# Optimization experiments

Measured on AMD Instinct MI355X. Metric: run time of the kernel, lower is better.

## Reference

```python
import jax, jax.numpy as jnp
import numpy as np

B, S, D, H, E = 4, 1024, 1024, 16, 4
HD = D // H
EPS = 1e-5


def setup_inputs() -> dict:
    key = jax.random.key(0)
    ks = jax.random.split(key, 6)
    std = 0.02
    return {
        "hidden_states": jax.random.normal(ks[0], (B, S, D), dtype=jnp.float32),
        "Wr": jax.random.normal(ks[1], (D, E), dtype=jnp.float32) * std,
        "br": jnp.zeros((E,), jnp.float32),
        "ln_g": jnp.ones((E, D), jnp.float32),
        "ln_b": jnp.zeros((E, D), jnp.float32),
        "W_attn": jax.random.normal(ks[2], (E, D, 3 * D), dtype=jnp.float32) * std,
        "b_attn": jnp.zeros((E, 3 * D), jnp.float32),
        "W_proj": jax.random.normal(ks[3], (E, D, D), dtype=jnp.float32) * std,
        "b_proj": jnp.zeros((E, D), jnp.float32),
    }


def reference(hidden_states, Wr, br, ln_g, ln_b, W_attn, b_attn, W_proj, b_proj):
    b, s, d = hidden_states.shape
    x = hidden_states.reshape(b * s, d)  # [N, D]

    # naive softmax router over experts
    score = jax.nn.softmax(x @ Wr + br, axis=-1)  # [N, E]

    # LayerNorm stats are expert-independent; affine is per-expert
    mu = jnp.mean(x, axis=-1, keepdims=True)
    var = jnp.mean(jnp.square(x - mu), axis=-1, keepdims=True)
    xn = (x - mu) * jax.lax.rsqrt(var + EPS)  # [N, D]

    ln_out = xn[:, None, :] * ln_g[None] + ln_b[None]  # [N, E, D]
    qkv_all = jnp.einsum('ned,edf->nef', ln_out, W_attn) + b_attn  # [N, E, 3D]
    # weighted_qkv: scale each expert's qkv by its routing score, sum
    qkv = jnp.einsum('ne,nef->nf', score, qkv_all)  # [N, 3D]

    q, k, v = jnp.split(qkv.reshape(b, s, 3 * d), 3, axis=-1)
    def split_heads(t):
        return t.reshape(b, s, H, HD).transpose(0, 2, 1, 3)  # [B,H,S,hd]
    q, k, v = split_heads(q), split_heads(k), split_heads(v)

    scale = 1.0 / jnp.sqrt(jnp.asarray(HD, q.dtype))
    att = jnp.einsum('bhqd,bhkd->bhqk', q, k) * scale  # [B,H,S,S]
    causal = jnp.tril(jnp.ones((s, s), dtype=bool))
    att = jnp.where(causal[None, None], att, jnp.finfo(att.dtype).min)
    probs = jax.nn.softmax(att, axis=-1)
    ctx = jnp.einsum('bhqk,bhkd->bhqd', probs, v)  # [B,H,S,hd]
    ctx = ctx.transpose(0, 2, 1, 3).reshape(b * s, d)  # [N, D]

    proj_all = jnp.einsum('nd,edf->nef', ctx, W_proj) + b_proj  # [N, E, D]
    out = jnp.einsum('ne,nef->nf', score, proj_all).reshape(b, s, d)
    return out
```

## Files before the change

kernel.cpp:

```cpp
#include <hip/hip_runtime.h>
#include <stdint.h>

#define NB 4
#define SS 1024
#define DD 1024
#define EE 4
#define HH 16
#define HDD 64
#define NN (NB*SS)
#define KK2 (EE*DD)
#define FF1 (3*DD)

typedef __attribute__((ext_vector_type(4))) float f32x4;
typedef __attribute__((ext_vector_type(8))) _Float16 half8;
typedef __attribute__((ext_vector_type(4))) _Float16 half4;

static __device__ __forceinline__ f32x4 mfma16(half8 a, half8 b, f32x4 c){
  return __builtin_amdgcn_mfma_f32_16x16x32_f16(a, b, c, 0, 0, 0);
}

#define GLOAD_LDS16(gp, lp) __builtin_amdgcn_global_load_lds( \
    (const unsigned int __attribute__((address_space(1)))*)(uintptr_t)(gp), \
    (unsigned int __attribute__((address_space(3)))*)(uintptr_t)(lp), 16, 0, 0)

#define SBAR() do { asm volatile("" ::: "memory"); \
                    __builtin_amdgcn_s_barrier(); \
                    asm volatile("" ::: "memory"); } while(0)

__global__ __launch_bounds__(256) void prep_kernel(
    const float* __restrict__ x, const float* __restrict__ Wr,
    const float* __restrict__ br, float* __restrict__ score,
    float* __restrict__ ratios, _Float16* __restrict__ xnb)
{
  int n = blockIdx.x;
  int tid = threadIdx.x;
  float4 xv = ((const float4*)(x + (size_t)n*DD))[tid];
  float xa[4] = {xv.x, xv.y, xv.z, xv.w};
  float vals[6];
  vals[0] = xa[0]+xa[1]+xa[2]+xa[3];
  vals[1] = xa[0]*xa[0]+xa[1]*xa[1]+xa[2]*xa[2]+xa[3]*xa[3];
  vals[2] = vals[3] = vals[4] = vals[5] = 0.f;
  #pragma unroll
  for (int j = 0; j < 4; ++j){
    float4 w = ((const float4*)Wr)[tid*4 + j];
    vals[2] += xa[j]*w.x; vals[3] += xa[j]*w.y;
    vals[4] += xa[j]*w.z; vals[5] += xa[j]*w.w;
  }
  #pragma unroll
  for (int off = 32; off >= 1; off >>= 1)
    #pragma unroll
    for (int i = 0; i < 6; ++i)
      vals[i] += __shfl_xor(vals[i], off, 64);
  __shared__ float red[4][6];
  int wid = tid >> 6;
  if ((tid & 63) == 0){
    #pragma unroll
    for (int i = 0; i < 6; ++i) red[wid][i] = vals[i];
  }
  __syncthreads();
  float tot[6];
  #pragma unroll
  for (int i = 0; i < 6; ++i)
    tot[i] = red[0][i] + red[1][i] + red[2][i] + red[3][i];

  float mu   = tot[0] * (1.f/DD);
  float var  = tot[1] * (1.f/DD) - mu*mu;
  float rsig = rsqrtf(var + 1e-5f);
  float lg[4];
  #pragma unroll
  for (int e = 0; e < 4; ++e) lg[e] = tot[2+e] + br[e];
  float mx = fmaxf(fmaxf(lg[0], lg[1]), fmaxf(lg[2], lg[3]));
  float ex[4], esum = 0.f;
  #pragma unroll
  for (int e = 0; e < 4; ++e){ ex[e] = __expf(lg[e] - mx); esum += ex[e]; }
  if (tid < 4){
    score[n*4 + tid] = ex[tid] / esum;
    ratios[n*4 + tid] = (tid > 0) ? (ex[tid-1] / ex[tid]) : 0.f;
  }

  half4 o;
  #pragma unroll
  for (int j = 0; j < 4; ++j) o[j] = (_Float16)((xa[j] - mu) * rsig);
  *(half4*)(xnb + (size_t)n*DD + tid*4) = o;
}

template<bool AFFINE>
__global__ __launch_bounds__(256) void transpose_f16_kernel(
    const float* __restrict__ W, _Float16* __restrict__ WT, int K, int F,
    const float* __restrict__ gvec, const float* __restrict__ bvec,
    float* __restrict__ part)
{
  __shared__ float t[64][65];
  __shared__ float red2[16][64];
  int k0 = blockIdx.x * 64, f0 = blockIdx.y * 64;
  int tid = threadIdx.x;
  int r = tid >> 4, c4 = (tid & 15) * 4;
  float pf[4] = {0.f, 0.f, 0.f, 0.f};
  #pragma unroll
  for (int i = 0; i < 4; ++i){
    int k = k0 + i*16 + r;
    float4 v = *(const float4*)(W + (size_t)k*F + f0 + c4);
    if constexpr (AFFINE){
      float bk = bvec[k];
      pf[0] += bk*v.x; pf[1] += bk*v.y; pf[2] += bk*v.z; pf[3] += bk*v.w;
      float gk = gvec[k];
      v.x *= gk; v.y *= gk; v.z *= gk; v.w *= gk;
    }
    t[i*16 + r][c4+0] = v.x; t[i*16 + r][c4+1] = v.y;
    t[i*16 + r][c4+2] = v.z; t[i*16 + r][c4+3] = v.w;
  }
  if constexpr (AFFINE){
    #pragma unroll
    for (int j = 0; j < 4; ++j) red2[r][c4+j] = pf[j];
  }
  __syncthreads();
  int f = tid >> 2, seg = tid & 3;
  half8 o0, o1;
  #pragma unroll
  for (int j = 0; j < 8; ++j){
    o0[j] = (_Float16)t[seg*16 + j][f];
    o1[j] = (_Float16)t[seg*16 + 8 + j][f];
  }
  _Float16* dst = WT + (size_t)(f0 + f)*K + k0 + seg*16;
  *(half8*)dst = o0;
  *(half8*)(dst + 8) = o1;
  if constexpr (AFFINE){
    if (tid < 64){
      float s = 0.f;
      #pragma unroll
      for (int rr = 0; rr < 16; ++rr) s += red2[rr][tid];
      part[(size_t)blockIdx.x * F + f0 + tid] = s;
    }
  }
}

__global__ __launch_bounds__(256) void bb1_kernel(
    const float* __restrict__ b_attn, const float* __restrict__ part,
    float* __restrict__ BB1)
{
  int idx = blockIdx.x*256 + threadIdx.x;
  int e = idx / FF1, f = idx - e*FF1;
  float s = b_attn[idx];
  #pragma unroll
  for (int i = 0; i < 16; ++i)
    s += part[(size_t)(e*16 + i)*FF1 + f];
  BB1[idx] = s;
}

#define G1_BM 256
#define G1_BN 192
#define G1_BK 64
#define G1_T  (KK2/G1_BK)
#define G1_ABUF (G1_BM*G1_BK)
#define G1_BBUF (G1_BN*G1_BK)
#define G1_BUFSZ (G1_ABUF+G1_BBUF)

__global__ __launch_bounds__(512, 2) void gemm1_kernel(
    const _Float16* __restrict__ XN, const _Float16* __restrict__ BT,
    const float* __restrict__ score, const float* __restrict__ ratios,
    const float* __restrict__ bias, _Float16* __restrict__ C)
{
  __shared__ _Float16 smem[2*G1_BUFSZ];
  int tid = threadIdx.x;
  int lane = tid & 63, wid = tid >> 6;
  int q = lane & 15, g = lane >> 4;
  int wr = wid >> 1, wc = wid & 1;
  int xo = (q & 7) << 3;
  int bid = blockIdx.x;
  int xcd = bid & 7, li = bid >> 3;
  int m0 = (li >> 1) * G1_BM;
  int n0 = (xcd*2 + (li & 1)) * G1_BN;

  int arow[4], brow[6];
  #pragma unroll
  for (int mf = 0; mf < 4; ++mf) arow[mf] = (wr*64 + mf*16 + q)*64;
  #pragma unroll
  for (int nf = 0; nf < 6; ++nf) brow[nf] = G1_ABUF + (wc*96 + nf*16 + q)*64;
  int soff[2] = { (g*8) ^ xo, (32 + g*8) ^ xo };

  auto stageA = [&](int t, int buf, int h){
    const int d0 = (t & 15) * G1_BK;
    _Float16* sA = smem + buf*G1_BUFSZ;
    #pragma unroll
    for (int ld = 0; ld < 2; ++ld){
      int l = h*2 + ld;
      int c = l*512 + tid;
      int row = c >> 3;
      int seg = (c & 7) ^ (row & 7);
      GLOAD_LDS16(XN + (size_t)(m0 + row)*DD + d0 + seg*8,
                  sA + (l*512 + wid*64)*8);
    }
  };
  auto stageB = [&](int t, int buf){
    const int k0 = t * G1_BK;
    _Float16* sB = smem + buf*G1_BUFSZ + G1_ABUF;
    #pragma unroll
    for (int ld = 0; ld < 3; ++ld){
      int c = ld*512 + tid;
      int row = c >> 3;
      int seg = (c & 7) ^ (row & 7);
      GLOAD_LDS16(BT + (size_t)(n0 + row)*KK2 + k0 + seg*8,
                  sB + (ld*512 + wid*64)*8);
    }
  };

  f32x4 acc[4][6] = {};
  half8 af0[2][2], af2[2][2], bf[6][2];

  stageA(0, 0, 0); stageA(0, 0, 1); stageB(0, 0);

  for (int t = 0; t < G1_T-1; ++t){
    if (t && (t & 15) == 0){
      int e = t >> 4;
      #pragma unroll
      for (int mf = 0; mf < 4; ++mf)
        #pragma unroll
        for (int r = 0; r < 4; ++r){
          int gm = m0 + wr*64 + mf*16 + g*4 + r;
          float ratio = ratios[gm*4 + e];
          #pragma unroll
          for (int nf = 0; nf < 6; ++nf)
            acc[mf][nf][r] *= ratio;
        }
    }
    int buf = t & 1, nxt = buf ^ 1;
    const _Float16* base = smem + buf*G1_BUFSZ;
    stageA(t+1, nxt, 0);
    asm volatile("s_waitcnt vmcnt(2)" ::: "memory");
    SBAR();
    #pragma unroll
    for (int m = 0; m < 2; ++m)
      #pragma unroll
      for (int k = 0; k < 2; ++k)
        af0[m][k] = *(const half8*)(base + arow[m] + soff[k]);
    #pragma unroll
    for (int n = 0; n < 3; ++n)
      #pragma unroll
      for (int k = 0; k < 2; ++k)
        bf[n][k] = *(const half8*)(base + brow[n] + soff[k]);
    stageA(t+1, nxt, 1);
    __builtin_amdgcn_s_setprio(1);
    #pragma unroll
    for (int k = 0; k < 2; ++k)
      #pragma unroll
      for (int m = 0; m < 2; ++m)
        #pragma unroll
        for (int n = 0; n < 3; ++n)
          acc[m][n] = mfma16(af0[m][k], bf[n][k], acc[m][n]);
    __builtin_amdgcn_s_setprio(0);
    SBAR();
    #pragma unroll
    for (int n = 3; n < 6; ++n)
      #pragma unroll
      for (int k = 0; k < 2; ++k)
        bf[n][k] = *(const half8*)(base + brow[n] + soff[k]);
    stageB(t+1, nxt);
    __builtin_amdgcn_s_setprio(1);
    #pragma unroll
    for (int k = 0; k < 2; ++k)
      #pragma unroll
      for (int m = 0; m < 2; ++m)
        #pragma unroll
        for (int n = 3; n < 6; ++n)
          acc[m][n] = mfma16(af0[m][k], bf[n][k], acc[m][n]);
    __builtin_amdgcn_s_setprio(0);
    SBAR();
    #pragma unroll
    for (int m = 0; m < 2; ++m)
      #pragma unroll
      for (int k = 0; k < 2; ++k)
        af2[m][k] = *(const half8*)(base + arow[2+m] + soff[k]);
    __builtin_amdgcn_s_setprio(1);
    #pragma unroll
    for (int k = 0; k < 2; ++k)
      #pragma unroll
      for (int m = 0; m < 2; ++m)
        #pragma unroll
        for (int n = 3; n < 6; ++n)
          acc[2+m][n] = mfma16(af2[m][k], bf[n][k], acc[2+m][n]);
    __builtin_amdgcn_s_setprio(0);
    SBAR();
    __builtin_amdgcn_s_setprio(1);
    #pragma unroll
    for (int k = 0; k < 2; ++k)
      #pragma unroll
      for (int m = 0; m < 2; ++m)
        #pragma unroll
        for (int n = 0; n < 3; ++n)
          acc[2+m][n] = mfma16(af2[m][k], bf[n][k], acc[2+m][n]);
    __builtin_amdgcn_s_setprio(0);
  }
  {
    const _Float16* base = smem + ((G1_T-1) & 1)*G1_BUFSZ;
    asm volatile("s_waitcnt vmcnt(0)" ::: "memory");
    SBAR();
    #pragma unroll
    for (int m = 0; m < 2; ++m)
      #pragma unroll
      for (int k = 0; k < 2; ++k){
        af0[m][k] = *(const half8*)(base + arow[m] + soff[k]);
        af2[m][k] = *(const half8*)(base + arow[2+m] + soff[k]);
      }
    #pragma unroll
    for (int n = 0; n < 6; ++n)
      #pragma unroll
      for (int k = 0; k < 2; ++k)
        bf[n][k] = *(const half8*)(base + brow[n] + soff[k]);
    #pragma unroll
    for (int k = 0; k < 2; ++k)
      #pragma unroll
      for (int m = 0; m < 2; ++m)
        #pragma unroll
        for (int n = 0; n < 6; ++n){
          acc[m][n]   = mfma16(af0[m][k], bf[n][k], acc[m][n]);
          acc[2+m][n] = mfma16(af2[m][k], bf[n][k], acc[2+m][n]);
        }
  }

  float bv[6][4];
  #pragma unroll
  for (int nf = 0; nf < 6; ++nf){
    int gn = n0 + wc*96 + nf*16 + q;
    #pragma unroll
    for (int e = 0; e < 4; ++e) bv[nf][e] = bias[e*FF1 + gn];
  }
  #pragma unroll
  for (int mf = 0; mf < 4; ++mf){
    #pragma unroll
    for (int r = 0; r < 4; ++r){
      int gm = m0 + wr*64 + mf*16 + g*4 + r;
      float4 sc = *(const float4*)(score + gm*4);
      #pragma unroll
      for (int nf = 0; nf < 6; ++nf){
        int gn = n0 + wc*96 + nf*16 + q;
        float v = acc[mf][nf][r]*sc.w
                + sc.x*bv[nf][0] + sc.y*bv[nf][1] + sc.z*bv[nf][2] + sc.w*bv[nf][3];
        C[(size_t)gm*FF1 + gn] = (_Float16)v;
      }
    }
  }
}

#define G2_BK 64
#define G2_ABUF (128*G2_BK)
#define G2_BUFSZ (2*G2_ABUF)

__global__ __launch_bounds__(512) void gemm2_kernel(
    const _Float16* __restrict__ CTX, const _Float16* __restrict__ BT,
    const float* __restrict__ score, const float* __restrict__ bias,
    float* __restrict__ Cout)
{
  __shared__ _Float16 smem[2*G2_BUFSZ];
  int tid = threadIdx.x;
  int lane = tid & 63, wid = tid >> 6;
  int q = lane & 15, g = lane >> 4;
  int wr = wid >> 2, wc = wid & 3;
  int xo = (q & 7) << 3;
  int bid = blockIdx.x;
  int xcd = bid >> 5, idx = bid & 31;
  int m0 = (xcd*4 + (idx >> 3)) * 128;
  int n0 = (idx & 7) * 128;

  int arow[4], brow[2];
  #pragma unroll
  for (int mf = 0; mf < 4; ++mf) arow[mf] = (wr*64 + mf*16 + q)*64;
  #pragma unroll
  for (int nf = 0; nf < 2; ++nf) brow[nf] = G2_ABUF + (wc*32 + nf*16 + q)*64;
  int soff[2] = { (g*8) ^ xo, (32 + g*8) ^ xo };

  auto stage = [&](int t, int buf){
    const int d0 = (t & 15) * G2_BK;
    const int k0 = t * G2_BK;
    _Float16* sA = smem + buf*G2_BUFSZ;
    _Float16* sB = sA + G2_ABUF;
    #pragma unroll
    for (int ld = 0; ld < 2; ++ld){
      int c = ld*512 + tid;
      int row = c >> 3;
      int seg = (c & 7) ^ (row & 7);
      GLOAD_LDS16(CTX + (size_t)(m0 + row)*DD + d0 + seg*8,
                  sA + (ld*512 + wid*64)*8);
    }
    #pragma unroll
    for (int ld = 0; ld < 2; ++ld){
      int c = ld*512 + tid;
      int row = c >> 3;
      int seg = (c & 7) ^ (row & 7);
      GLOAD_LDS16(BT + (size_t)(n0 + row)*KK2 + k0 + seg*8,
                  sB + (ld*512 + wid*64)*8);
    }
  };

  f32x4 accp[4][2] = {}, acco[4][2] = {};

  auto compute = [&](int buf){
    const _Float16* base = smem + buf*G2_BUFSZ;
    half8 af[4][2], bfr[2][2];
    #pragma unroll
    for (int m = 0; m < 4; ++m)
      #pragma unroll
      for (int k = 0; k < 2; ++k)
        af[m][k] = *(const half8*)(base + arow[m] + soff[k]);
    #pragma unroll
    for (int n = 0; n < 2; ++n)
      #pragma unroll
      for (int k = 0; k < 2; ++k)
        bfr[n][k] = *(const half8*)(base + brow[n] + soff[k]);
    __builtin_amdgcn_s_setprio(1);
    #pragma unroll
    for (int k = 0; k < 2; ++k)
      #pragma unroll
      for (int m = 0; m < 4; ++m)
        #pragma unroll
        for (int n = 0; n < 2; ++n)
          accp[m][n] = mfma16(af[m][k], bfr[n][k], accp[m][n]);
    __builtin_amdgcn_s_setprio(0);
  };

  auto merge = [&](int e){
    #pragma unroll
    for (int m = 0; m < 4; ++m)
      #pragma unroll
      for (int r = 0; r < 4; ++r){
        int gm = m0 + wr*64 + m*16 + g*4 + r;
        float s = score[(size_t)gm*4 + e];
        #pragma unroll
        for (int n = 0; n < 2; ++n){
          acco[m][n][r] += s*accp[m][n][r];
          accp[m][n][r] = 0.f;
        }
      }
  };

  stage(0, 0);
  for (int t = 0; t < KK2/G2_BK - 1; ++t){
    stage(t+1, (t+1)&1);
    asm volatile("s_waitcnt vmcnt(4)" ::: "memory");
    SBAR();
    compute(t & 1);
    SBAR();
    if ((t & 15) == 15) merge(t >> 4);
  }
  asm volatile("s_waitcnt vmcnt(0)" ::: "memory");
  SBAR();
  compute((KK2/G2_BK - 1) & 1);
  merge(3);

  #pragma unroll
  for (int m = 0; m < 4; ++m){
    #pragma unroll
    for (int r = 0; r < 4; ++r){
      int gm = m0 + wr*64 + m*16 + g*4 + r;
      float4 sc = *(const float4*)(score + gm*4);
      #pragma unroll
      for (int n = 0; n < 2; ++n){
        int gn = n0 + wc*32 + n*16 + q;
        float v = acco[m][n][r]
                + sc.x*bias[gn] + sc.y*bias[DD+gn]
                + sc.z*bias[2*DD+gn] + sc.w*bias[3*DD+gn];
        Cout[(size_t)gm*DD + gn] = v;
      }
    }
  }
}

__global__ __launch_bounds__(256) void attn_kernel(
    const _Float16* __restrict__ qkv, _Float16* __restrict__ ctx)
{
  __shared__ _Float16 lsK[2][64*64];
  __shared__ _Float16 lsV[2][64*64];
  __shared__ _Float16 lsP[4][16*64];
  int bh = blockIdx.x, qt = blockIdx.y;
  int b = bh >> 4, h = bh & 15;
  int tid = threadIdx.x, lane = tid & 63, wid = tid >> 6;
  int q = lane & 15, g = lane >> 4;
  int xo = (q & 7) << 3;
  int qrow0 = qt*64 + wid*16;

  half8 qf[2];
  #pragma unroll
  for (int kk = 0; kk < 2; ++kk)
    qf[kk] = *(const half8*)(qkv + ((size_t)b*SS + qrow0 + q)*FF1 + h*HDD + kk*32 + g*8);

  auto issueK = [&](int kt, int buf){
    size_t kvrow = (size_t)b*SS + kt*64;
    #pragma unroll
    for (int i = 0; i < 2; ++i){
      int c = i*256 + tid;
      int row = c >> 3, seg = (c & 7) ^ (row & 7);
      GLOAD_LDS16(qkv + (kvrow + row)*FF1 + DD + h*HDD + seg*8,
                  lsK[buf] + (size_t)(i*256 + wid*64)*8);
    }
  };
  auto issueV = [&](int kt, half8* vr){
    size_t kvrow = (size_t)b*SS + kt*64;
    #pragma unroll
    for (int i = 0; i < 2; ++i)
      vr[i] = *(const half8*)(qkv + (kvrow + lane)*FF1 + 2*DD + h*HDD + (wid*2+i)*8);
  };
  auto writeV = [&](const half8* vr, int buf){
    #pragma unroll
    for (int i = 0; i < 2; ++i){
      int p = wid*2 + i;
      #pragma unroll
      for (int j = 0; j < 8; ++j){
        int hd = p*8 + j;
        lsV[buf][hd*64 + (lane ^ ((hd & 7) << 3))] = vr[i][j];
      }
    }
  };

  f32x4 o[4] = {};
  float mrow = -1e30f, lsum = 0.f;
  const float SC2 = 0.18033688011112042f;
  int qglob = qrow0 + q;

  half8 vr[2];
  issueK(0, 0);
  issueV(0, vr);

  for (int kt = 0; kt <= qt; ++kt){
    int cur = kt & 1, nxt = cur ^ 1;
    int tn = (kt < qt) ? kt+1 : qt;
    asm volatile("s_waitcnt vmcnt(2)" ::: "memory");
    SBAR();

    f32x4 st[4] = {};
    #pragma unroll
    for (int i = 0; i < 4; ++i){
      #pragma unroll
      for (int kk = 0; kk < 2; ++kk){
        half8 kf = *(const half8*)(lsK[cur] + (i*16 + q)*64 + ((kk*32 + g*8) ^ xo));
        st[i] = mfma16(kf, qf[kk], st[i]);
      }
    }
    issueK(tn, nxt);
    asm volatile("s_waitcnt vmcnt(2)" ::: "memory");
    writeV(vr, cur);

    float pvv[16]; float tm = -1e30f;
    #pragma unroll
    for (int i = 0; i < 4; ++i)
      #pragma unroll
      for (int r = 0; r < 4; ++r){
        int kglob = kt*64 + i*16 + g*4 + r;
        float sv = (kglob <= qglob) ? st[i][r]*SC2 : -1e30f;
        pvv[i*4+r] = sv; tm = fmaxf(tm, sv);
      }
    tm = fmaxf(tm, __shfl_xor(tm, 16, 64));
    tm = fmaxf(tm, __shfl_xor(tm, 32, 64));
    float mnew  = fmaxf(mrow, tm);
    float alpha = exp2f(mrow - mnew);
    mrow = mnew;
    float psum = 0.f;
    _Float16 pb[16];
    #pragma unroll
    for (int i = 0; i < 16; ++i){
      float p = exp2f(pvv[i] - mnew);
      psum += p; pb[i] = (_Float16)p;
    }
    lsum = lsum*alpha + psum;
    float af4[4];
    #pragma unroll
    for (int r = 0; r < 4; ++r) af4[r] = __shfl(alpha, g*4 + r, 64);
    #pragma unroll
    for (int n = 0; n < 4; ++n)
      #pragma unroll
      for (int r = 0; r < 4; ++r) o[n][r] *= af4[r];
    issueV(tn, vr);

    asm volatile("s_waitcnt lgkmcnt(0)" ::: "memory");
    SBAR();

    #pragma unroll
    for (int i = 0; i < 4; ++i){
      half4 w4;
      w4[0]=pb[i*4+0]; w4[1]=pb[i*4+1]; w4[2]=pb[i*4+2]; w4[3]=pb[i*4+3];
      *(half4*)(&lsP[wid][q*64 + ((i*16 + g*4) ^ xo)]) = w4;
    }
    #pragma unroll
    for (int kk = 0; kk < 2; ++kk){
      half8 pf = *(const half8*)(&lsP[wid][q*64 + ((kk*32 + g*8) ^ xo)]);
      #pragma unroll
      for (int n = 0; n < 4; ++n){
        half8 vf = *(const half8*)(&lsV[cur][(n*16 + q)*64 + ((kk*32 + g*8) ^ xo)]);
        o[n] = mfma16(pf, vf, o[n]);
      }
    }
  }
  float lt = lsum + __shfl_xor(lsum, 16, 64);
  lt = lt + __shfl_xor(lt, 32, 64);
  float rinv = 1.f / lt;
  #pragma unroll
  for (int r = 0; r < 4; ++r){
    float ri = __shfl(rinv, g*4 + r, 64);
    int qg = qt*64 + wid*16 + g*4 + r;
    _Float16* obase = ctx + ((size_t)b*SS + qg)*DD + h*HDD;
    #pragma unroll
    for (int n = 0; n < 4; ++n)
      obase[n*16 + q] = (_Float16)(o[n][r] * ri);
  }
}

extern "C" void kernel_launch(void* const* d_in, const int* in_sizes, int n_in,
                              void* d_out, int out_size, void* d_ws, size_t ws_size,
                              hipStream_t stream)
{
  const float* x      = (const float*)d_in[0];
  const float* Wr     = (const float*)d_in[1];
  const float* br     = (const float*)d_in[2];
  const float* ln_g   = (const float*)d_in[3];
  const float* ln_b   = (const float*)d_in[4];
  const float* W_attn = (const float*)d_in[5];
  const float* b_attn = (const float*)d_in[6];
  const float* W_proj = (const float*)d_in[7];
  const float* b_proj = (const float*)d_in[8];
  (void)in_sizes; (void)n_in; (void)out_size; (void)ws_size;

  char* ws = (char*)d_ws;
  size_t off = 0;
  auto alloc = [&](size_t bytes) -> void* {
    void* p = ws + off; off += (bytes + 255) & ~(size_t)255; return p;
  };
  _Float16* W1gT  = (_Float16*)alloc((size_t)FF1*KK2*2);
  _Float16* W2T   = (_Float16*)alloc((size_t)DD*KK2*2);
  float*    score = (float*)   alloc((size_t)NN*4*4);
  float*    ratio = (float*)   alloc((size_t)NN*4*4);
  _Float16* xn16  = (_Float16*)alloc((size_t)NN*DD*2);
  _Float16* qkv   = (_Float16*)alloc((size_t)NN*FF1*2);
  _Float16* ctx   = (_Float16*)alloc((size_t)NN*DD*2);
  float*    part  = (float*)   alloc((size_t)(KK2/64)*FF1*4);
  float*    BB1   = (float*)   alloc((size_t)EE*FF1*4);

  hipLaunchKernelGGL((transpose_f16_kernel<true>), dim3(KK2/64, FF1/64), dim3(256), 0, stream,
                     W_attn, W1gT, KK2, FF1, ln_g, ln_b, part);
  hipLaunchKernelGGL((transpose_f16_kernel<false>), dim3(KK2/64, DD/64), dim3(256), 0, stream,
                     W_proj, W2T, KK2, DD, nullptr, nullptr, nullptr);
  hipLaunchKernelGGL(bb1_kernel, dim3(EE*FF1/256), dim3(256), 0, stream,
                     b_attn, part, BB1);
  hipLaunchKernelGGL(prep_kernel, dim3(NN), dim3(256), 0, stream,
                     x, Wr, br, score, ratio, xn16);
  hipLaunchKernelGGL(gemm1_kernel, dim3(256), dim3(512), 0, stream,
                     xn16, W1gT, score, ratio, BB1, qkv);
  hipLaunchKernelGGL(attn_kernel, dim3(NB*HH, SS/64), dim3(256), 0, stream,
                     qkv, ctx);
  hipLaunchKernelGGL(gemm2_kernel, dim3(256), dim3(512), 0, stream,
                     ctx, W2T, score, b_proj, (float*)d_out);
}
```

Measured before the change: 206.8 us.

## Enlarge attention query tile to 128 rows and restructure GEMM barrier placement

The attention kernel now uses 512 threads per block, covering 128 query rows per block. Each 64-row K/V tile loaded into LDS is therefore reused by eight waves instead of four, and each thread issues one K and one V load per tile. In gemm1 several barriers are moved later or removed so LDS reads overlap with MFMAs, and gemm2's compute is split by k-half with one barrier interleaved. Risks are LDS races from moved barriers and wasted causal work on the diagonal tiles of larger blocks.

```diff
diff --git a/kernel.cpp b/kernel.cpp
--- a/kernel.cpp
+++ b/kernel.cpp
@@ -248,13 +248,13 @@
         for (int n = 0; n < 3; ++n)
           acc[m][n] = mfma16(af0[m][k], bf[n][k], acc[m][n]);
     __builtin_amdgcn_s_setprio(0);
-    SBAR();
     #pragma unroll
     for (int n = 3; n < 6; ++n)
       #pragma unroll
       for (int k = 0; k < 2; ++k)
         bf[n][k] = *(const half8*)(base + brow[n] + soff[k]);
     stageB(t+1, nxt);
+    SBAR();
     __builtin_amdgcn_s_setprio(1);
     #pragma unroll
     for (int k = 0; k < 2; ++k)
@@ -264,12 +264,12 @@
         for (int n = 3; n < 6; ++n)
           acc[m][n] = mfma16(af0[m][k], bf[n][k], acc[m][n]);
     __builtin_amdgcn_s_setprio(0);
-    SBAR();
     #pragma unroll
     for (int m = 0; m < 2; ++m)
       #pragma unroll
       for (int k = 0; k < 2; ++k)
         af2[m][k] = *(const half8*)(base + arow[2+m] + soff[k]);
+    SBAR();
     __builtin_amdgcn_s_setprio(1);
     #pragma unroll
     for (int k = 0; k < 2; ++k)
@@ -278,9 +278,6 @@
         #pragma unroll
         for (int n = 3; n < 6; ++n)
           acc[2+m][n] = mfma16(af2[m][k], bf[n][k], acc[2+m][n]);
-    __builtin_amdgcn_s_setprio(0);
-    SBAR();
-    __builtin_amdgcn_s_setprio(1);
     #pragma unroll
     for (int k = 0; k < 2; ++k)
       #pragma unroll
@@ -393,30 +390,6 @@
 
   f32x4 accp[4][2] = {}, acco[4][2] = {};
 
-  auto compute = [&](int buf){
-    const _Float16* base = smem + buf*G2_BUFSZ;
-    half8 af[4][2], bfr[2][2];
-    #pragma unroll
-    for (int m = 0; m < 4; ++m)
-      #pragma unroll
-      for (int k = 0; k < 2; ++k)
-        af[m][k] = *(const half8*)(base + arow[m] + soff[k]);
-    #pragma unroll
-    for (int n = 0; n < 2; ++n)
-      #pragma unroll
-      for (int k = 0; k < 2; ++k)
-        bfr[n][k] = *(const half8*)(base + brow[n] + soff[k]);
-    __builtin_amdgcn_s_setprio(1);
-    #pragma unroll
-    for (int k = 0; k < 2; ++k)
-      #pragma unroll
-      for (int m = 0; m < 4; ++m)
-        #pragma unroll
-        for (int n = 0; n < 2; ++n)
-          accp[m][n] = mfma16(af[m][k], bfr[n][k], accp[m][n]);
-    __builtin_amdgcn_s_setprio(0);
-  };
-
   auto merge = [&](int e){
     #pragma unroll
     for (int m = 0; m < 4; ++m)
@@ -432,19 +405,46 @@
       }
   };
 
+  half8 af[4][2], bfr[2][2];
+  auto reads = [&](const _Float16* base, int k){
+    #pragma unroll
+    for (int m = 0; m < 4; ++m)
+      af[m][k] = *(const half8*)(base + arow[m] + soff[k]);
+    #pragma unroll
+    for (int n = 0; n < 2; ++n)
+      bfr[n][k] = *(const half8*)(base + brow[n] + soff[k]);
+  };
+  auto mfmas = [&](int k){
+    __builtin_amdgcn_s_setprio(1);
+    #pragma unroll
+    for (int m = 0; m < 4; ++m)
+      #pragma unroll
+      for (int n = 0; n < 2; ++n)
+        accp[m][n] = mfma16(af[m][k], bfr[n][k], accp[m][n]);
+    __builtin_amdgcn_s_setprio(0);
+  };
+
   stage(0, 0);
   for (int t = 0; t < KK2/G2_BK - 1; ++t){
+    const _Float16* base = smem + (t & 1)*G2_BUFSZ;
     stage(t+1, (t+1)&1);
     asm volatile("s_waitcnt vmcnt(4)" ::: "memory");
     SBAR();
-    compute(t & 1);
-    SBAR();
+    reads(base, 0);
+    mfmas(0);
+    reads(base, 1);
+    SBAR();
+    mfmas(1);
     if ((t & 15) == 15) merge(t >> 4);
   }
-  asm volatile("s_waitcnt vmcnt(0)" ::: "memory");
-  SBAR();
-  compute((KK2/G2_BK - 1) & 1);
-  merge(3);
+  {
+    const _Float16* base = smem + ((KK2/G2_BK - 1) & 1)*G2_BUFSZ;
+    asm volatile("s_waitcnt vmcnt(0)" ::: "memory");
+    SBAR();
+    reads(base, 0); reads(base, 1);
+    mfmas(0); mfmas(1);
+    merge(3);
+  }
 
   #pragma unroll
   for (int m = 0; m < 4; ++m){
@@ -464,18 +464,18 @@
   }
 }
 
-__global__ __launch_bounds__(256) void attn_kernel(
+__global__ __launch_bounds__(512) void attn_kernel(
     const _Float16* __restrict__ qkv, _Float16* __restrict__ ctx)
 {
   __shared__ _Float16 lsK[2][64*64];
   __shared__ _Float16 lsV[2][64*64];
-  __shared__ _Float16 lsP[4][16*64];
+  __shared__ _Float16 lsP[8][16*64];
   int bh = blockIdx.x, qt = blockIdx.y;
   int b = bh >> 4, h = bh & 15;
   int tid = threadIdx.x, lane = tid & 63, wid = tid >> 6;
   int q = lane & 15, g = lane >> 4;
   int xo = (q & 7) << 3;
-  int qrow0 = qt*64 + wid*16;
+  int qrow0 = qt*128 + wid*16;
 
   half8 qf[2];
   #pragma unroll
@@ -484,29 +484,19 @@
 
   auto issueK = [&](int kt, int buf){
     size_t kvrow = (size_t)b*SS + kt*64;
-    #pragma unroll
-    for (int i = 0; i < 2; ++i){
-      int c = i*256 + tid;
-      int row = c >> 3, seg = (c & 7) ^ (row & 7);
-      GLOAD_LDS16(qkv + (kvrow + row)*FF1 + DD + h*HDD + seg*8,
-                  lsK[buf] + (size_t)(i*256 + wid*64)*8);
-    }
-  };
-  auto issueV = [&](int kt, half8* vr){
+    int row = tid >> 3, seg = (tid & 7) ^ (row & 7);
+    GLOAD_LDS16(qkv + (kvrow + row)*FF1 + DD + h*HDD + seg*8,
+                lsK[buf] + (size_t)(wid*64)*8);
+  };
+  auto issueV = [&](int kt, half8& vr){
     size_t kvrow = (size_t)b*SS + kt*64;
-    #pragma unroll
-    for (int i = 0; i < 2; ++i)
-      vr[i] = *(const half8*)(qkv + (kvrow + lane)*FF1 + 2*DD + h*HDD + (wid*2+i)*8);
-  };
-  auto writeV = [&](const half8* vr, int buf){
-    #pragma unroll
-    for (int i = 0; i < 2; ++i){
-      int p = wid*2 + i;
-      #pragma unroll
-      for (int j = 0; j < 8; ++j){
-        int hd = p*8 + j;
-        lsV[buf][hd*64 + (lane ^ ((hd & 7) << 3))] = vr[i][j];
-      }
+    vr = *(const half8*)(qkv + (kvrow + lane)*FF1 + 2*DD + h*HDD + wid*8);
+  };
+  auto writeV = [&](half8 vr, int buf){
+    #pragma unroll
+    for (int j = 0; j < 8; ++j){
+      int hd = wid*8 + j;
+      lsV[buf][hd*64 + (lane ^ ((hd & 7) << 3))] = vr[j];
     }
   };
 
@@ -514,15 +504,16 @@
   float mrow = -1e30f, lsum = 0.f;
   const float SC2 = 0.18033688011112042f;
   int qglob = qrow0 + q;
-
-  half8 vr[2];
+  int ktmax = 2*qt + 1;
+
+  half8 vr;
   issueK(0, 0);
   issueV(0, vr);
 
-  for (int kt = 0; kt <= qt; ++kt){
+  for (int kt = 0; kt <= ktmax; ++kt){
     int cur = kt & 1, nxt = cur ^ 1;
-    int tn = (kt < qt) ? kt+1 : qt;
-    asm volatile("s_waitcnt vmcnt(2)" ::: "memory");
+    int tn = (kt < ktmax) ? kt+1 : ktmax;
+    asm volatile("s_waitcnt vmcnt(1)" ::: "memory");
     SBAR();
 
     f32x4 st[4] = {};
@@ -535,7 +526,7 @@
       }
     }
     issueK(tn, nxt);
-    asm volatile("s_waitcnt vmcnt(2)" ::: "memory");
+    asm volatile("s_waitcnt vmcnt(1)" ::: "memory");
     writeV(vr, cur);
 
     float pvv[16]; float tm = -1e30f;
@@ -594,7 +585,7 @@
   #pragma unroll
   for (int r = 0; r < 4; ++r){
     float ri = __shfl(rinv, g*4 + r, 64);
-    int qg = qt*64 + wid*16 + g*4 + r;
+    int qg = qt*128 + wid*16 + g*4 + r;
     _Float16* obase = ctx + ((size_t)b*SS + qg)*DD + h*HDD;
     #pragma unroll
     for (int n = 0; n < 4; ++n)
@@ -642,7 +633,7 @@
                      x, Wr, br, score, ratio, xn16);
   hipLaunchKernelGGL(gemm1_kernel, dim3(256), dim3(512), 0, stream,
                      xn16, W1gT, score, ratio, BB1, qkv);
-  hipLaunchKernelGGL(attn_kernel, dim3(NB*HH, SS/64), dim3(256), 0, stream,
+  hipLaunchKernelGGL(attn_kernel, dim3(NB*HH, SS/128), dim3(512), 0, stream,
                      qkv, ctx);
   hipLaunchKernelGGL(gemm2_kernel, dim3(256), dim3(512), 0, stream,
                      ctx, W2T, score, b_proj, (float*)d_out);
```

Measured after the change: 199.8 us. 1.04x faster.
